# Performance work log

Measured on AMD Instinct MI355X. Metric: run time of the kernel, lower is better.

## Reference

```python
import jax, jax.numpy as jnp
import numpy as np

N_ENTS = 50000
N_EDGES = 500000
N_RELS = 200
RANK = 128
N_LAYERS = 2
RRELU_SLOPE = (1.0 / 8.0 + 1.0 / 3.0) / 2.0  # F.rrelu eval-mode: mean of default lower/upper


def setup_inputs() -> dict:
    key = jax.random.key(0)
    ks = jax.random.split(key, 9)
    return {
        "ent_emb": jax.random.normal(ks[0], (N_ENTS, RANK), dtype=jnp.float32),
        "rel_emb": jax.random.normal(ks[1], (N_RELS, RANK), dtype=jnp.float32),
        "norm": jax.random.uniform(ks[2], (N_ENTS, 1), dtype=jnp.float32),
        "Wn": jax.random.normal(ks[3], (N_LAYERS, RANK, RANK), dtype=jnp.float32) * 0.05,
        "Wl": jax.random.normal(ks[4], (N_LAYERS, RANK, RANK), dtype=jnp.float32) * 0.05,
        "Wa": jax.random.normal(ks[5], (N_LAYERS, RANK, RANK), dtype=jnp.float32) * 0.05,
        "src": jax.random.randint(ks[6], (N_EDGES,), 0, N_ENTS, dtype=jnp.int32),
        "dst": jax.random.randint(ks[7], (N_EDGES,), 0, N_ENTS, dtype=jnp.int32),
        "etype": jax.random.randint(ks[8], (N_EDGES,), 0, N_RELS, dtype=jnp.int32),
    }


def reference(ent_emb, rel_emb, norm, Wn, Wl, Wa, src, dst, etype):
    n = ent_emb.shape[0]
    # in-degree mask (same graph across layers)
    in_deg = jax.ops.segment_sum(jnp.ones_like(dst, dtype=jnp.float32), dst, num_segments=n)
    has_in = (in_deg > 0)[:, None]  # [N,1]
    h = ent_emb
    for l in range(Wn.shape[0]):
        # edge gather + add + linear: msg = (h[src] + rel_emb[etype]) @ Wn[l]
        msg = (h[src] + rel_emb[etype]) @ Wn[l]  # [E, rank]
        # scatter-sum into destination nodes, then per-node norm
        agg = jax.ops.segment_sum(msg, dst, num_segments=n) * norm  # [N, rank]
        # masked self-loop: loop_weight where in_degree>0, else alone_loop_weight
        loop = jnp.where(has_in, h @ Wl[l], h @ Wa[l])
        h = agg + loop
        # rrelu in eval mode == leaky relu with slope (1/8 + 1/3)/2
        h = jnp.where(h >= 0, h, h * RRELU_SLOPE)
        # dropout=0.0 -> identity
    return h
```

## Files before the change

kernel.cpp:

```cpp
#include <hip/hip_runtime.h>

#define SLOPE 0.22916666666666666f
#define ALONE_CAP 2048

typedef __attribute__((ext_vector_type(8))) short bfrag;
typedef __attribute__((ext_vector_type(4))) float ffrag;

__device__ __forceinline__ unsigned short rne16(float f) {
    unsigned u = __float_as_uint(f);
    return (unsigned short)((u + 0x7FFFu + ((u >> 16) & 1u)) >> 16);
}
__device__ __forceinline__ float bf2f(unsigned short h) {
    return __uint_as_float(((unsigned)h) << 16);
}

__global__ __launch_bounds__(256) void prep_kernel(
    const int* __restrict__ dst, int* __restrict__ deg, int e, int eb,
    const float* __restrict__ ent, ushort* __restrict__ Eh, ushort* __restrict__ El,
    int total4, int cb,
    const float* __restrict__ Wn, const float* __restrict__ Wl,
    ushort* __restrict__ packW) {
    int b = blockIdx.x;
    if (b < eb) {
        int i = b * 256 + threadIdx.x;
        if (i < e) atomicAdd(&deg[dst[i]], 1);
    } else if (b < eb + cb) {
        int i = (b - eb) * 256 + threadIdx.x;
        if (i >= total4) return;
        float4 v = ((const float4*)ent)[i];
        ushort4 hi, lo;
        hi.x = rne16(v.x); lo.x = rne16(v.x - bf2f(hi.x));
        hi.y = rne16(v.y); lo.y = rne16(v.y - bf2f(hi.y));
        hi.z = rne16(v.z); lo.z = rne16(v.z - bf2f(hi.z));
        hi.w = rne16(v.w); lo.w = rne16(v.w - bf2f(hi.w));
        ((ushort4*)Eh)[i] = hi;
        ((ushort4*)El)[i] = lo;
    } else {
        int t = (b - eb - cb) * 256 + threadIdx.x;
        if (t >= 4 * 4 * 128 * 4) return;
        int quad = t & 3;
        int nn   = (t >> 2) & 127;
        int kc   = (t >> 9) & 3;
        int mat  = t >> 11;
        const float* W = ((mat & 1) ? Wl : Wn) + (mat >> 1) * 16384;
        ushort* oh = packW + mat * 32768;
        ushort* ol = oh + 16384;
        int obase = ((kc * 128 + nn) * 4 + quad) * 8;
        #pragma unroll
        for (int j = 0; j < 8; ++j) {
            float w = W[(kc * 32 + quad * 8 + j) * 128 + nn];
            unsigned short hi = rne16(w);
            oh[obase + j] = hi;
            ol[obase + j] = rne16(w - bf2f(hi));
        }
    }
}

__global__ __launch_bounds__(256) void scan_partial_kernel(const int* __restrict__ deg,
                                                           int* __restrict__ partial, int n) {
    __shared__ int wsum[4];
    int base = blockIdx.x * 1024;
    int t = threadIdx.x;
    int s = 0;
    #pragma unroll
    for (int j = 0; j < 4; ++j) {
        int i = base + t + 256 * j;
        if (i < n) s += deg[i];
    }
    #pragma unroll
    for (int off = 1; off < 64; off <<= 1) s += __shfl_xor(s, off, 64);
    if ((t & 63) == 0) wsum[t >> 6] = s;
    __syncthreads();
    if (t == 0) partial[blockIdx.x] = wsum[0] + wsum[1] + wsum[2] + wsum[3];
}

__global__ __launch_bounds__(64) void scan_aux_kernel(int* __restrict__ partial, int nparts) {
    int t = threadIdx.x;
    int v = (t < nparts) ? partial[t] : 0;
    int x = v;
    #pragma unroll
    for (int off = 1; off < 64; off <<= 1) {
        int y = __shfl_up(x, off, 64);
        if (t >= off) x += y;
    }
    if (t < nparts) partial[t] = x - v;
}

__global__ __launch_bounds__(256) void scan_final_kernel(const int* __restrict__ deg,
                                                         const int* __restrict__ partial,
                                                         int* __restrict__ row_off,
                                                         int* __restrict__ alone_list,
                                                         int* __restrict__ alone_count, int n) {
    __shared__ int wsum[4];
    int base = blockIdx.x * 1024;
    int t = threadIdx.x, lane = t & 63, wid = t >> 6;
    int i0 = base + t * 4;
    int v0 = (i0 + 0 < n) ? deg[i0 + 0] : 0;
    int v1 = (i0 + 1 < n) ? deg[i0 + 1] : 0;
    int v2 = (i0 + 2 < n) ? deg[i0 + 2] : 0;
    int v3 = (i0 + 3 < n) ? deg[i0 + 3] : 0;
    int s = v0 + v1 + v2 + v3;
    int x = s;
    #pragma unroll
    for (int off = 1; off < 64; off <<= 1) {
        int y = __shfl_up(x, off, 64);
        if (lane >= off) x += y;
    }
    if (lane == 63) wsum[wid] = x;
    __syncthreads();
    int wbase = 0;
    #pragma unroll
    for (int w = 0; w < 4; ++w) { int ws = wsum[w]; if (w < wid) wbase += ws; }
    int p = partial[blockIdx.x] + wbase + x - s;
    if (i0 + 0 <= n) row_off[i0 + 0] = p;
    p += v0;
    if (i0 + 1 <= n) row_off[i0 + 1] = p;
    p += v1;
    if (i0 + 2 <= n) row_off[i0 + 2] = p;
    p += v2;
    if (i0 + 3 <= n) row_off[i0 + 3] = p;
    if (i0 + 0 < n && v0 == 0) { int q = atomicAdd(alone_count, 1); if (q < ALONE_CAP) alone_list[q] = i0; }
    if (i0 + 1 < n && v1 == 0) { int q = atomicAdd(alone_count, 1); if (q < ALONE_CAP) alone_list[q] = i0 + 1; }
    if (i0 + 2 < n && v2 == 0) { int q = atomicAdd(alone_count, 1); if (q < ALONE_CAP) alone_list[q] = i0 + 2; }
    if (i0 + 3 < n && v3 == 0) { int q = atomicAdd(alone_count, 1); if (q < ALONE_CAP) alone_list[q] = i0 + 3; }
}

__global__ __launch_bounds__(256) void scatter_kernel(
    const int* __restrict__ src, const int* __restrict__ dst,
    const int* __restrict__ ety, const int* __restrict__ row_off,
    int* __restrict__ cursor, unsigned* __restrict__ edges, int e) {
    int i = blockIdx.x * 256 + threadIdx.x;
    if (i < e) {
        int v = dst[i];
        int pos = row_off[v] + atomicAdd(&cursor[v], 1);
        edges[pos] = (unsigned)src[i] | ((unsigned)ety[i] << 16);
    }
}

__global__ __launch_bounds__(256) void agg_kernel(
    const float* __restrict__ h, const float* __restrict__ rel,
    const float* __restrict__ norm, const int* __restrict__ row_off,
    const unsigned* __restrict__ edges, ushort* __restrict__ Sh,
    ushort* __restrict__ Sl, int n) {
    int wave = threadIdx.x >> 6, lane = threadIdx.x & 63;
    int v = blockIdx.x * 4 + wave;
    if (v >= n) return;
    int s0 = row_off[v], s1 = row_off[v + 1];
    float nm = norm[v];
    int half = lane >> 5;
    int c4 = (lane & 31) * 4;
    float4 acc = make_float4(0.f, 0.f, 0.f, 0.f);
    int e = s0;
    for (; e + 3 < s1; e += 4) {
        unsigned q0 = edges[e + half];
        unsigned q1 = edges[e + 2 + half];
        const float4* ha0 = (const float4*)&h[(size_t)(q0 & 0xFFFFu) * 128 + c4];
        const float4* ra0 = (const float4*)&rel[(size_t)(q0 >> 16) * 128 + c4];
        const float4* ha1 = (const float4*)&h[(size_t)(q1 & 0xFFFFu) * 128 + c4];
        const float4* ra1 = (const float4*)&rel[(size_t)(q1 >> 16) * 128 + c4];
        float4 h0 = *ha0, r0 = *ra0, h1 = *ha1, r1 = *ra1;
        acc.x += (h0.x + r0.x) + (h1.x + r1.x);
        acc.y += (h0.y + r0.y) + (h1.y + r1.y);
        acc.z += (h0.z + r0.z) + (h1.z + r1.z);
        acc.w += (h0.w + r0.w) + (h1.w + r1.w);
    }
    for (; e + 1 < s1; e += 2) {
        unsigned q0 = edges[e + half];
        float4 h0 = *(const float4*)&h[(size_t)(q0 & 0xFFFFu) * 128 + c4];
        float4 r0 = *(const float4*)&rel[(size_t)(q0 >> 16) * 128 + c4];
        acc.x += h0.x + r0.x; acc.y += h0.y + r0.y;
        acc.z += h0.z + r0.z; acc.w += h0.w + r0.w;
    }
    if (e < s1 && half == 0) {
        unsigned q0 = edges[e];
        float4 h0 = *(const float4*)&h[(size_t)(q0 & 0xFFFFu) * 128 + c4];
        float4 r0 = *(const float4*)&rel[(size_t)(q0 >> 16) * 128 + c4];
        acc.x += h0.x + r0.x; acc.y += h0.y + r0.y;
        acc.z += h0.z + r0.z; acc.w += h0.w + r0.w;
    }
    acc.x += __shfl_xor(acc.x, 32, 64);
    acc.y += __shfl_xor(acc.y, 32, 64);
    acc.z += __shfl_xor(acc.z, 32, 64);
    acc.w += __shfl_xor(acc.w, 32, 64);
    if (half == 0) {
        acc.x *= nm; acc.y *= nm; acc.z *= nm; acc.w *= nm;
        ushort4 hi, lo;
        hi.x = rne16(acc.x); lo.x = rne16(acc.x - bf2f(hi.x));
        hi.y = rne16(acc.y); lo.y = rne16(acc.y - bf2f(hi.y));
        hi.z = rne16(acc.z); lo.z = rne16(acc.z - bf2f(hi.z));
        hi.w = rne16(acc.w); lo.w = rne16(acc.w - bf2f(hi.w));
        *(ushort4*)&Sh[(size_t)v * 128 + c4] = hi;
        *(ushort4*)&Sl[(size_t)v * 128 + c4] = lo;
    }
}

__global__ __launch_bounds__(256) void gemm_mfma_kernel(
    const ushort* __restrict__ Sh, const ushort* __restrict__ Sl,
    const ushort* Hh, const ushort* Hl,
    const ushort* __restrict__ Pnh, const ushort* __restrict__ Pnl,
    const ushort* __restrict__ Plh, const ushort* __restrict__ Pll,
    float* __restrict__ out, ushort* Oh, ushort* Ol, int n) {
    const int tid = threadIdx.x;
    const int wave = tid >> 6, lane = tid & 63;
    const int quad = lane >> 4, l16 = lane & 15;
    const int wr = wave >> 1, wc = wave & 1;
    const int row_base = blockIdx.x * 64 + wr * 32;
    const int col_base = wc * 64;

    int r0c = row_base + l16;       if (r0c > n - 1) r0c = n - 1;
    int r1c = row_base + 16 + l16;  if (r1c > n - 1) r1c = n - 1;

    int colc[4];
    #pragma unroll
    for (int ct = 0; ct < 4; ++ct) colc[ct] = col_base + ct * 16 + l16;

    ffrag acc[2][4];
    #pragma unroll
    for (int rt = 0; rt < 2; ++rt)
        #pragma unroll
        for (int ct = 0; ct < 4; ++ct) acc[rt][ct] = (ffrag)0.f;

    #pragma unroll 1
    for (int half = 0; half < 2; ++half) {
        const ushort* Ah = half ? Hh : Sh;
        const ushort* Al = half ? Hl : Sl;
        const ushort* Pbh = half ? Plh : Pnh;
        const ushort* Pbl = half ? Pll : Pnl;
        #pragma unroll 1
        for (int kc = 0; kc < 4; ++kc) {
            const int koff = kc * 32 + quad * 8;
            bfrag ah[2], al[2], bh[4], bl[4];
            ah[0] = *(const bfrag*)(Ah + (size_t)r0c * 128 + koff);
            ah[1] = *(const bfrag*)(Ah + (size_t)r1c * 128 + koff);
            al[0] = *(const bfrag*)(Al + (size_t)r0c * 128 + koff);
            al[1] = *(const bfrag*)(Al + (size_t)r1c * 128 + koff);
            #pragma unroll
            for (int ct = 0; ct < 4; ++ct) {
                int bidx = ((kc * 128 + colc[ct]) * 4 + quad) * 8;
                bh[ct] = *(const bfrag*)(Pbh + bidx);
                bl[ct] = *(const bfrag*)(Pbl + bidx);
            }
            #pragma unroll
            for (int rt = 0; rt < 2; ++rt)
                #pragma unroll
                for (int ct = 0; ct < 4; ++ct)
                    acc[rt][ct] = __builtin_amdgcn_mfma_f32_16x16x32_bf16(
                        ah[rt], bh[ct], acc[rt][ct], 0, 0, 0);
            #pragma unroll
            for (int rt = 0; rt < 2; ++rt)
                #pragma unroll
                for (int ct = 0; ct < 4; ++ct)
                    acc[rt][ct] = __builtin_amdgcn_mfma_f32_16x16x32_bf16(
                        ah[rt], bl[ct], acc[rt][ct], 0, 0, 0);
            #pragma unroll
            for (int rt = 0; rt < 2; ++rt)
                #pragma unroll
                for (int ct = 0; ct < 4; ++ct)
                    acc[rt][ct] = __builtin_amdgcn_mfma_f32_16x16x32_bf16(
                        al[rt], bh[ct], acc[rt][ct], 0, 0, 0);
        }
    }

    __syncthreads();

    #pragma unroll
    for (int rt = 0; rt < 2; ++rt) {
        #pragma unroll
        for (int ct = 0; ct < 4; ++ct) {
            #pragma unroll
            for (int rg = 0; rg < 4; ++rg) {
                int r = row_base + rt * 16 + quad * 4 + rg;
                if (r < n) {
                    int c = colc[ct];
                    float v = acc[rt][ct][rg];
                    v = v >= 0.f ? v : v * SLOPE;
                    out[(size_t)r * 128 + c] = v;
                    if (Oh) {
                        unsigned short hi = rne16(v);
                        Oh[(size_t)r * 128 + c] = hi;
                        Ol[(size_t)r * 128 + c] = rne16(v - bf2f(hi));
                    }
                }
            }
        }
    }
}

__global__ __launch_bounds__(128) void fixup_kernel(
    const float* __restrict__ Hrows, int by_node,
    const float* __restrict__ Wa,
    const int* __restrict__ alone_list, const int* __restrict__ alone_count,
    float* out, ushort* Oh, ushort* Ol, float* asave) {
    int cnt = *alone_count;
    if (cnt > ALONE_CAP) cnt = ALONE_CAP;
    int t = threadIdx.x;
    for (int i = blockIdx.x; i < cnt; i += gridDim.x) {
        int v = alone_list[i];
        const float* hrow = Hrows + (size_t)(by_node ? v : i) * 128;
        float acc = 0.f;
        for (int k = 0; k < 128; ++k)
            acc += hrow[k] * Wa[k * 128 + t];
        float o = acc >= 0.f ? acc : acc * SLOPE;
        out[(size_t)v * 128 + t] = o;
        if (Oh) {
            unsigned short hi = rne16(o);
            Oh[(size_t)v * 128 + t] = hi;
            Ol[(size_t)v * 128 + t] = rne16(o - bf2f(hi));
        }
        if (asave) asave[(size_t)i * 128 + t] = o;
    }
}

extern "C" void kernel_launch(void* const* d_in, const int* in_sizes, int n_in,
                              void* d_out, int out_size, void* d_ws, size_t ws_size,
                              hipStream_t stream) {
    const float* ent  = (const float*)d_in[0];
    const float* rel  = (const float*)d_in[1];
    const float* norm = (const float*)d_in[2];
    const float* Wn   = (const float*)d_in[3];
    const float* Wl   = (const float*)d_in[4];
    const float* Wa   = (const float*)d_in[5];
    const int*   src  = (const int*)d_in[6];
    const int*   dst  = (const int*)d_in[7];
    const int*   ety  = (const int*)d_in[8];
    float* out = (float*)d_out;

    const int n = in_sizes[2];
    const int e = in_sizes[7];

    char* ws = (char*)d_ws;
    int* deg         = (int*)ws;
    int* cursor      = deg + n;
    int* alone_count = cursor + n;
    size_t zbytes = (size_t)(2 * n + 1) * sizeof(int);
    size_t p = (zbytes + 255) & ~(size_t)255;
    int* row_off = (int*)(ws + p);
    p += (((size_t)(n + 1) * 4) + 255) & ~(size_t)255;
    int* partial = (int*)(ws + p);
    p += 256;
    int* alone_list = (int*)(ws + p);
    p += (((size_t)ALONE_CAP * 4) + 255) & ~(size_t)255;
    float* asave = (float*)(ws + p);
    p += (((size_t)ALONE_CAP * 128 * 4) + 255) & ~(size_t)255;
    unsigned* edges = (unsigned*)(ws + p);
    p += (((size_t)e * 4) + 255) & ~(size_t)255;
    ushort* Sh = (ushort*)(ws + p);
    p += (((size_t)n * 128 * 2) + 255) & ~(size_t)255;
    ushort* Sl = (ushort*)(ws + p);
    p += (((size_t)n * 128 * 2) + 255) & ~(size_t)255;
    ushort* Eh = (ushort*)(ws + p);
    p += (((size_t)n * 128 * 2) + 255) & ~(size_t)255;
    ushort* El = (ushort*)(ws + p);
    p += (((size_t)n * 128 * 2) + 255) & ~(size_t)255;
    ushort* packW = (ushort*)(ws + p);
    p += 4 * 32768 * 2;
    float* h1 = out;

    const int eb = (e + 255) / 256;
    const int cb = (n * 32 + 255) / 256;
    const int nparts = (n + 1023) / 1024;
    const int gb = (n + 63) / 64;
    const int ab = (n + 3) / 4;

    hipMemsetAsync(ws, 0, zbytes, stream);
    prep_kernel<<<eb + cb + 32, 256, 0, stream>>>(dst, deg, e, eb,
                                                  ent, Eh, El, n * 32, cb,
                                                  Wn, Wl, packW);
    scan_partial_kernel<<<nparts, 256, 0, stream>>>(deg, partial, n);
    scan_aux_kernel<<<1, 64, 0, stream>>>(partial, nparts);
    scan_final_kernel<<<nparts, 256, 0, stream>>>(deg, partial, row_off,
                                                  alone_list, alone_count, n);
    scatter_kernel<<<eb, 256, 0, stream>>>(src, dst, ety, row_off, cursor, edges, e);

    agg_kernel<<<ab, 256, 0, stream>>>(ent, rel, norm, row_off, edges, Sh, Sl, n);
    gemm_mfma_kernel<<<gb, 256, 0, stream>>>(Sh, Sl, Eh, El,
                                             packW, packW + 16384,
                                             packW + 32768, packW + 49152,
                                             h1, Eh, El, n);
    fixup_kernel<<<16, 128, 0, stream>>>(ent, 1, Wa, alone_list, alone_count,
                                         h1, Eh, El, asave);

    agg_kernel<<<ab, 256, 0, stream>>>(h1, rel, norm, row_off, edges, Sh, Sl, n);
    gemm_mfma_kernel<<<gb, 256, 0, stream>>>(Sh, Sl, Eh, El,
                                             packW + 65536, packW + 81920,
                                             packW + 98304, packW + 114688,
                                             out, nullptr, nullptr, n);
    fixup_kernel<<<16, 128, 0, stream>>>(asave, 0, Wa + 16384, alone_list, alone_count,
                                         out, nullptr, nullptr, nullptr);
}
```

Before: 307.1 us.

## Interleave hi/lo bf16 splits, fuse scan aux, widen GEMM waves, unroll gather by 8

Hi and lo bf16 halves now sit together in one 32-bit word per element, for entity features, aggregated sums and layer-1 output. This cuts separate array traffic and lets layer 2 gather from the split buffer instead of the fp32 h1. The scan aux kernel is removed; each final-scan block sums the partials before it, which saves a launch. The GEMM now uses 128-thread blocks in which each wave computes all 128 columns. The edge gather loop is unrolled to 8 edges for more memory-level parallelism. Layer 1 no longer writes fp32 output.

```diff
diff --git a/kernel.cpp b/kernel.cpp
--- a/kernel.cpp
+++ b/kernel.cpp
@@ -13,10 +13,21 @@
 __device__ __forceinline__ float bf2f(unsigned short h) {
     return __uint_as_float(((unsigned)h) << 16);
 }
+__device__ __forceinline__ unsigned packsplit(float f) {
+    unsigned short hi = rne16(f);
+    unsigned short lo = rne16(f - bf2f(hi));
+    return ((unsigned)hi << 16) | lo;
+}
+__device__ __forceinline__ float recon(unsigned u) {
+    return __uint_as_float(u & 0xFFFF0000u) + __uint_as_float(u << 16);
+}
+__device__ __forceinline__ float4 recon4(uint4 u) {
+    return make_float4(recon(u.x), recon(u.y), recon(u.z), recon(u.w));
+}
 
 __global__ __launch_bounds__(256) void prep_kernel(
     const int* __restrict__ dst, int* __restrict__ deg, int e, int eb,
-    const float* __restrict__ ent, ushort* __restrict__ Eh, ushort* __restrict__ El,
+    const float* __restrict__ ent, unsigned* __restrict__ Esp,
     int total4, int cb,
     const float* __restrict__ Wn, const float* __restrict__ Wl,
     ushort* __restrict__ packW) {
@@ -28,13 +39,10 @@
         int i = (b - eb) * 256 + threadIdx.x;
         if (i >= total4) return;
         float4 v = ((const float4*)ent)[i];
-        ushort4 hi, lo;
-        hi.x = rne16(v.x); lo.x = rne16(v.x - bf2f(hi.x));
-        hi.y = rne16(v.y); lo.y = rne16(v.y - bf2f(hi.y));
-        hi.z = rne16(v.z); lo.z = rne16(v.z - bf2f(hi.z));
-        hi.w = rne16(v.w); lo.w = rne16(v.w - bf2f(hi.w));
-        ((ushort4*)Eh)[i] = hi;
-        ((ushort4*)El)[i] = lo;
+        uint4 w;
+        w.x = packsplit(v.x); w.y = packsplit(v.y);
+        w.z = packsplit(v.z); w.w = packsplit(v.w);
+        ((uint4*)Esp)[i] = w;
     } else {
         int t = (b - eb - cb) * 256 + threadIdx.x;
         if (t >= 4 * 4 * 128 * 4) return;
@@ -74,26 +82,22 @@
     if (t == 0) partial[blockIdx.x] = wsum[0] + wsum[1] + wsum[2] + wsum[3];
 }
 
-__global__ __launch_bounds__(64) void scan_aux_kernel(int* __restrict__ partial, int nparts) {
-    int t = threadIdx.x;
-    int v = (t < nparts) ? partial[t] : 0;
-    int x = v;
-    #pragma unroll
-    for (int off = 1; off < 64; off <<= 1) {
-        int y = __shfl_up(x, off, 64);
-        if (t >= off) x += y;
-    }
-    if (t < nparts) partial[t] = x - v;
-}
-
 __global__ __launch_bounds__(256) void scan_final_kernel(const int* __restrict__ deg,
                                                          const int* __restrict__ partial,
                                                          int* __restrict__ row_off,
                                                          int* __restrict__ alone_list,
                                                          int* __restrict__ alone_count, int n) {
     __shared__ int wsum[4];
-    int base = blockIdx.x * 1024;
+    __shared__ int sbase;
+    int bid = blockIdx.x;
     int t = threadIdx.x, lane = t & 63, wid = t >> 6;
+    if (wid == 0) {
+        int v = (lane < bid) ? partial[lane] : 0;
+        #pragma unroll
+        for (int off = 1; off < 64; off <<= 1) v += __shfl_xor(v, off, 64);
+        if (lane == 0) sbase = v;
+    }
+    int base = bid * 1024;
     int i0 = base + t * 4;
     int v0 = (i0 + 0 < n) ? deg[i0 + 0] : 0;
     int v1 = (i0 + 1 < n) ? deg[i0 + 1] : 0;
@@ -111,7 +115,7 @@
     int wbase = 0;
     #pragma unroll
     for (int w = 0; w < 4; ++w) { int ws = wsum[w]; if (w < wid) wbase += ws; }
-    int p = partial[blockIdx.x] + wbase + x - s;
+    int p = sbase + wbase + x - s;
     if (i0 + 0 <= n) row_off[i0 + 0] = p;
     p += v0;
     if (i0 + 1 <= n) row_off[i0 + 1] = p;
@@ -137,11 +141,12 @@
     }
 }
 
+template <int SPLIT>
 __global__ __launch_bounds__(256) void agg_kernel(
-    const float* __restrict__ h, const float* __restrict__ rel,
+    const float* __restrict__ hf, const unsigned* __restrict__ hs,
+    const float* __restrict__ rel,
     const float* __restrict__ norm, const int* __restrict__ row_off,
-    const unsigned* __restrict__ edges, ushort* __restrict__ Sh,
-    ushort* __restrict__ Sl, int n) {
+    const unsigned* __restrict__ edges, unsigned* __restrict__ Ssp, int n) {
     int wave = threadIdx.x >> 6, lane = threadIdx.x & 63;
     int v = blockIdx.x * 4 + wave;
     if (v >= n) return;
@@ -151,29 +156,44 @@
     int c4 = (lane & 31) * 4;
     float4 acc = make_float4(0.f, 0.f, 0.f, 0.f);
     int e = s0;
-    for (; e + 3 < s1; e += 4) {
+    for (; e + 7 < s1; e += 8) {
         unsigned q0 = edges[e + half];
         unsigned q1 = edges[e + 2 + half];
-        const float4* ha0 = (const float4*)&h[(size_t)(q0 & 0xFFFFu) * 128 + c4];
-        const float4* ra0 = (const float4*)&rel[(size_t)(q0 >> 16) * 128 + c4];
-        const float4* ha1 = (const float4*)&h[(size_t)(q1 & 0xFFFFu) * 128 + c4];
-        const float4* ra1 = (const float4*)&rel[(size_t)(q1 >> 16) * 128 + c4];
-        float4 h0 = *ha0, r0 = *ra0, h1 = *ha1, r1 = *ra1;
-        acc.x += (h0.x + r0.x) + (h1.x + r1.x);
-        acc.y += (h0.y + r0.y) + (h1.y + r1.y);
-        acc.z += (h0.z + r0.z) + (h1.z + r1.z);
-        acc.w += (h0.w + r0.w) + (h1.w + r1.w);
+        unsigned q2 = edges[e + 4 + half];
+        unsigned q3 = edges[e + 6 + half];
+        float4 h0, h1, h2, h3;
+        if (SPLIT) {
+            h0 = recon4(*(const uint4*)&hs[(size_t)(q0 & 0xFFFFu) * 128 + c4]);
+            h1 = recon4(*(const uint4*)&hs[(size_t)(q1 & 0xFFFFu) * 128 + c4]);
+            h2 = recon4(*(const uint4*)&hs[(size_t)(q2 & 0xFFFFu) * 128 + c4]);
+            h3 = recon4(*(const uint4*)&hs[(size_t)(q3 & 0xFFFFu) * 128 + c4]);
+        } else {
+            h0 = *(const float4*)&hf[(size_t)(q0 & 0xFFFFu) * 128 + c4];
+            h1 = *(const float4*)&hf[(size_t)(q1 & 0xFFFFu) * 128 + c4];
+            h2 = *(const float4*)&hf[(size_t)(q2 & 0xFFFFu) * 128 + c4];
+            h3 = *(const float4*)&hf[(size_t)(q3 & 0xFFFFu) * 128 + c4];
+        }
+        float4 r0 = *(const float4*)&rel[(size_t)(q0 >> 16) * 128 + c4];
+        float4 r1 = *(const float4*)&rel[(size_t)(q1 >> 16) * 128 + c4];
+        float4 r2 = *(const float4*)&rel[(size_t)(q2 >> 16) * 128 + c4];
+        float4 r3 = *(const float4*)&rel[(size_t)(q3 >> 16) * 128 + c4];
+        acc.x += ((h0.x + r0.x) + (h1.x + r1.x)) + ((h2.x + r2.x) + (h3.x + r3.x));
+        acc.y += ((h0.y + r0.y) + (h1.y + r1.y)) + ((h2.y + r2.y) + (h3.y + r3.y));
+        acc.z += ((h0.z + r0.z) + (h1.z + r1.z)) + ((h2.z + r2.z) + (h3.z + r3.z));
+        acc.w += ((h0.w + r0.w) + (h1.w + r1.w)) + ((h2.w + r2.w) + (h3.w + r3.w));
     }
     for (; e + 1 < s1; e += 2) {
         unsigned q0 = edges[e + half];
-        float4 h0 = *(const float4*)&h[(size_t)(q0 & 0xFFFFu) * 128 + c4];
+        float4 h0 = SPLIT ? recon4(*(const uint4*)&hs[(size_t)(q0 & 0xFFFFu) * 128 + c4])
+                          : *(const float4*)&hf[(size_t)(q0 & 0xFFFFu) * 128 + c4];
         float4 r0 = *(const float4*)&rel[(size_t)(q0 >> 16) * 128 + c4];
         acc.x += h0.x + r0.x; acc.y += h0.y + r0.y;
         acc.z += h0.z + r0.z; acc.w += h0.w + r0.w;
     }
     if (e < s1 && half == 0) {
         unsigned q0 = edges[e];
-        float4 h0 = *(const float4*)&h[(size_t)(q0 & 0xFFFFu) * 128 + c4];
+        float4 h0 = SPLIT ? recon4(*(const uint4*)&hs[(size_t)(q0 & 0xFFFFu) * 128 + c4])
+                          : *(const float4*)&hf[(size_t)(q0 & 0xFFFFu) * 128 + c4];
         float4 r0 = *(const float4*)&rel[(size_t)(q0 >> 16) * 128 + c4];
         acc.x += h0.x + r0.x; acc.y += h0.y + r0.y;
         acc.z += h0.z + r0.z; acc.w += h0.w + r0.w;
@@ -183,79 +203,79 @@
     acc.z += __shfl_xor(acc.z, 32, 64);
     acc.w += __shfl_xor(acc.w, 32, 64);
     if (half == 0) {
-        acc.x *= nm; acc.y *= nm; acc.z *= nm; acc.w *= nm;
-        ushort4 hi, lo;
-        hi.x = rne16(acc.x); lo.x = rne16(acc.x - bf2f(hi.x));
-        hi.y = rne16(acc.y); lo.y = rne16(acc.y - bf2f(hi.y));
-        hi.z = rne16(acc.z); lo.z = rne16(acc.z - bf2f(hi.z));
-        hi.w = rne16(acc.w); lo.w = rne16(acc.w - bf2f(hi.w));
-        *(ushort4*)&Sh[(size_t)v * 128 + c4] = hi;
-        *(ushort4*)&Sl[(size_t)v * 128 + c4] = lo;
-    }
-}
-
-__global__ __launch_bounds__(256) void gemm_mfma_kernel(
-    const ushort* __restrict__ Sh, const ushort* __restrict__ Sl,
-    const ushort* Hh, const ushort* Hl,
+        uint4 w;
+        w.x = packsplit(acc.x * nm); w.y = packsplit(acc.y * nm);
+        w.z = packsplit(acc.z * nm); w.w = packsplit(acc.w * nm);
+        *(uint4*)&Ssp[(size_t)v * 128 + c4] = w;
+    }
+}
+
+__global__ __launch_bounds__(128) void gemm_mfma_kernel(
+    const unsigned* __restrict__ Ssp, const unsigned* Hsp,
     const ushort* __restrict__ Pnh, const ushort* __restrict__ Pnl,
     const ushort* __restrict__ Plh, const ushort* __restrict__ Pll,
-    float* __restrict__ out, ushort* Oh, ushort* Ol, int n) {
+    float* __restrict__ out, unsigned* Osp, int n) {
     const int tid = threadIdx.x;
     const int wave = tid >> 6, lane = tid & 63;
     const int quad = lane >> 4, l16 = lane & 15;
-    const int wr = wave >> 1, wc = wave & 1;
-    const int row_base = blockIdx.x * 64 + wr * 32;
-    const int col_base = wc * 64;
+    const int row_base = blockIdx.x * 64 + wave * 32;
 
     int r0c = row_base + l16;       if (r0c > n - 1) r0c = n - 1;
     int r1c = row_base + 16 + l16;  if (r1c > n - 1) r1c = n - 1;
 
-    int colc[4];
-    #pragma unroll
-    for (int ct = 0; ct < 4; ++ct) colc[ct] = col_base + ct * 16 + l16;
-
-    ffrag acc[2][4];
+    ffrag acc[2][8];
     #pragma unroll
     for (int rt = 0; rt < 2; ++rt)
         #pragma unroll
-        for (int ct = 0; ct < 4; ++ct) acc[rt][ct] = (ffrag)0.f;
+        for (int ct = 0; ct < 8; ++ct) acc[rt][ct] = (ffrag)0.f;
 
     #pragma unroll 1
     for (int half = 0; half < 2; ++half) {
-        const ushort* Ah = half ? Hh : Sh;
-        const ushort* Al = half ? Hl : Sl;
+        const unsigned* A = half ? Hsp : Ssp;
         const ushort* Pbh = half ? Plh : Pnh;
         const ushort* Pbl = half ? Pll : Pnl;
         #pragma unroll 1
         for (int kc = 0; kc < 4; ++kc) {
             const int koff = kc * 32 + quad * 8;
-            bfrag ah[2], al[2], bh[4], bl[4];
-            ah[0] = *(const bfrag*)(Ah + (size_t)r0c * 128 + koff);
-            ah[1] = *(const bfrag*)(Ah + (size_t)r1c * 128 + koff);
-            al[0] = *(const bfrag*)(Al + (size_t)r0c * 128 + koff);
-            al[1] = *(const bfrag*)(Al + (size_t)r1c * 128 + koff);
-            #pragma unroll
-            for (int ct = 0; ct < 4; ++ct) {
-                int bidx = ((kc * 128 + colc[ct]) * 4 + quad) * 8;
+            uint4 a0a = *(const uint4*)(A + (size_t)r0c * 128 + koff);
+            uint4 a0b = *(const uint4*)(A + (size_t)r0c * 128 + koff + 4);
+            uint4 a1a = *(const uint4*)(A + (size_t)r1c * 128 + koff);
+            uint4 a1b = *(const uint4*)(A + (size_t)r1c * 128 + koff + 4);
+            bfrag ah[2], al[2];
+            #pragma unroll
+            for (int j = 0; j < 4; ++j) {
+                unsigned u0 = ((const unsigned*)&a0a)[j];
+                unsigned u1 = ((const unsigned*)&a0b)[j];
+                ah[0][j]     = (short)(u0 >> 16); al[0][j]     = (short)(u0 & 0xFFFFu);
+                ah[0][j + 4] = (short)(u1 >> 16); al[0][j + 4] = (short)(u1 & 0xFFFFu);
+                unsigned u2 = ((const unsigned*)&a1a)[j];
+                unsigned u3 = ((const unsigned*)&a1b)[j];
+                ah[1][j]     = (short)(u2 >> 16); al[1][j]     = (short)(u2 & 0xFFFFu);
+                ah[1][j + 4] = (short)(u3 >> 16); al[1][j + 4] = (short)(u3 & 0xFFFFu);
+            }
+            bfrag bh[8], bl[8];
+            #pragma unroll
+            for (int ct = 0; ct < 8; ++ct) {
+                int bidx = ((kc * 128 + ct * 16 + l16) * 4 + quad) * 8;
                 bh[ct] = *(const bfrag*)(Pbh + bidx);
                 bl[ct] = *(const bfrag*)(Pbl + bidx);
             }
             #pragma unroll
             for (int rt = 0; rt < 2; ++rt)
                 #pragma unroll
-                for (int ct = 0; ct < 4; ++ct)
+                for (int ct = 0; ct < 8; ++ct)
                     acc[rt][ct] = __builtin_amdgcn_mfma_f32_16x16x32_bf16(
                         ah[rt], bh[ct], acc[rt][ct], 0, 0, 0);
             #pragma unroll
             for (int rt = 0; rt < 2; ++rt)
                 #pragma unroll
-                for (int ct = 0; ct < 4; ++ct)
+                for (int ct = 0; ct < 8; ++ct)
                     acc[rt][ct] = __builtin_amdgcn_mfma_f32_16x16x32_bf16(
                         ah[rt], bl[ct], acc[rt][ct], 0, 0, 0);
             #pragma unroll
             for (int rt = 0; rt < 2; ++rt)
                 #pragma unroll
-                for (int ct = 0; ct < 4; ++ct)
+                for (int ct = 0; ct < 8; ++ct)
                     acc[rt][ct] = __builtin_amdgcn_mfma_f32_16x16x32_bf16(
                         al[rt], bh[ct], acc[rt][ct], 0, 0, 0);
         }
@@ -266,20 +286,16 @@
     #pragma unroll
     for (int rt = 0; rt < 2; ++rt) {
         #pragma unroll
-        for (int ct = 0; ct < 4; ++ct) {
+        for (int ct = 0; ct < 8; ++ct) {
             #pragma unroll
             for (int rg = 0; rg < 4; ++rg) {
                 int r = row_base + rt * 16 + quad * 4 + rg;
                 if (r < n) {
-                    int c = colc[ct];
+                    int c = ct * 16 + l16;
                     float v = acc[rt][ct][rg];
                     v = v >= 0.f ? v : v * SLOPE;
-                    out[(size_t)r * 128 + c] = v;
-                    if (Oh) {
-                        unsigned short hi = rne16(v);
-                        Oh[(size_t)r * 128 + c] = hi;
-                        Ol[(size_t)r * 128 + c] = rne16(v - bf2f(hi));
-                    }
+                    if (out) out[(size_t)r * 128 + c] = v;
+                    if (Osp) Osp[(size_t)r * 128 + c] = packsplit(v);
                 }
             }
         }
@@ -290,7 +306,7 @@
     const float* __restrict__ Hrows, int by_node,
     const float* __restrict__ Wa,
     const int* __restrict__ alone_list, const int* __restrict__ alone_count,
-    float* out, ushort* Oh, ushort* Ol, float* asave) {
+    float* out, unsigned* Osp, float* asave) {
     int cnt = *alone_count;
     if (cnt > ALONE_CAP) cnt = ALONE_CAP;
     int t = threadIdx.x;
@@ -301,12 +317,8 @@
         for (int k = 0; k < 128; ++k)
             acc += hrow[k] * Wa[k * 128 + t];
         float o = acc >= 0.f ? acc : acc * SLOPE;
-        out[(size_t)v * 128 + t] = o;
-        if (Oh) {
-            unsigned short hi = rne16(o);
-            Oh[(size_t)v * 128 + t] = hi;
-            Ol[(size_t)v * 128 + t] = rne16(o - bf2f(hi));
-        }
+        if (out) out[(size_t)v * 128 + t] = o;
+        if (Osp) Osp[(size_t)v * 128 + t] = packsplit(o);
         if (asave) asave[(size_t)i * 128 + t] = o;
     }
 }
@@ -344,17 +356,12 @@
     p += (((size_t)ALONE_CAP * 128 * 4) + 255) & ~(size_t)255;
     unsigned* edges = (unsigned*)(ws + p);
     p += (((size_t)e * 4) + 255) & ~(size_t)255;
-    ushort* Sh = (ushort*)(ws + p);
-    p += (((size_t)n * 128 * 2) + 255) & ~(size_t)255;
-    ushort* Sl = (ushort*)(ws + p);
-    p += (((size_t)n * 128 * 2) + 255) & ~(size_t)255;
-    ushort* Eh = (ushort*)(ws + p);
-    p += (((size_t)n * 128 * 2) + 255) & ~(size_t)255;
-    ushort* El = (ushort*)(ws + p);
-    p += (((size_t)n * 128 * 2) + 255) & ~(size_t)255;
+    unsigned* Ssp = (unsigned*)(ws + p);
+    p += (((size_t)n * 128 * 4) + 255) & ~(size_t)255;
+    unsigned* Esp = (unsigned*)(ws + p);
+    p += (((size_t)n * 128 * 4) + 255) & ~(size_t)255;
     ushort* packW = (ushort*)(ws + p);
     p += 4 * 32768 * 2;
-    float* h1 = out;
 
     const int eb = (e + 255) / 256;
     const int cb = (n * 32 + 255) / 256;
@@ -364,27 +371,26 @@
 
     hipMemsetAsync(ws, 0, zbytes, stream);
     prep_kernel<<<eb + cb + 32, 256, 0, stream>>>(dst, deg, e, eb,
-                                                  ent, Eh, El, n * 32, cb,
+                                                  ent, Esp, n * 32, cb,
                                                   Wn, Wl, packW);
     scan_partial_kernel<<<nparts, 256, 0, stream>>>(deg, partial, n);
-    scan_aux_kernel<<<1, 64, 0, stream>>>(partial, nparts);
     scan_final_kernel<<<nparts, 256, 0, stream>>>(deg, partial, row_off,
                                                   alone_list, alone_count, n);
     scatter_kernel<<<eb, 256, 0, stream>>>(src, dst, ety, row_off, cursor, edges, e);
 
-    agg_kernel<<<ab, 256, 0, stream>>>(ent, rel, norm, row_off, edges, Sh, Sl, n);
-    gemm_mfma_kernel<<<gb, 256, 0, stream>>>(Sh, Sl, Eh, El,
+    agg_kernel<0><<<ab, 256, 0, stream>>>(ent, nullptr, rel, norm, row_off, edges, Ssp, n);
+    gemm_mfma_kernel<<<gb, 128, 0, stream>>>(Ssp, Esp,
                                              packW, packW + 16384,
                                              packW + 32768, packW + 49152,
-                                             h1, Eh, El, n);
+                                             nullptr, Esp, n);
     fixup_kernel<<<16, 128, 0, stream>>>(ent, 1, Wa, alone_list, alone_count,
-                                         h1, Eh, El, asave);
-
-    agg_kernel<<<ab, 256, 0, stream>>>(h1, rel, norm, row_off, edges, Sh, Sl, n);
-    gemm_mfma_kernel<<<gb, 256, 0, stream>>>(Sh, Sl, Eh, El,
+                                         nullptr, Esp, asave);
+
+    agg_kernel<1><<<ab, 256, 0, stream>>>(nullptr, Esp, rel, norm, row_off, edges, Ssp, n);
+    gemm_mfma_kernel<<<gb, 128, 0, stream>>>(Ssp, Esp,
                                              packW + 65536, packW + 81920,
                                              packW + 98304, packW + 114688,
-                                             out, nullptr, nullptr, n);
+                                             out, nullptr, n);
     fixup_kernel<<<16, 128, 0, stream>>>(asave, 0, Wa + 16384, alone_list, alone_count,
-                                         out, nullptr, nullptr, nullptr);
-}
+                                         out, nullptr, nullptr);
+}
```

Result: faster. 294.1 us (-4.3%).
